# Optimization experiments

Measured on AMD Instinct MI355X. Metric: run time of the kernel, lower is better.

The kernel has to match this reference:

```python
import jax, jax.numpy as jnp
import numpy as np

N, D, K = 131072, 768, 2000


def setup_inputs() -> dict:
    key = jax.random.key(0)
    kx, kc = jax.random.split(key)
    x = jax.random.normal(kx, (N, D), dtype=jnp.float32)
    centroids = jax.random.normal(kc, (D, K), dtype=jnp.float32)  # stored as [D, K] like the torch module
    return {"x": x, "centroids": centroids}


def reference(x, centroids):
    # dist[n,k] = ||x_n||^2 - 2 x_n . c_k + ||c_k||^2  (matmul trick)
    x_norm = jnp.sum(x * x, axis=1, keepdims=True)              # [N, 1]
    c_norm = jnp.sum(centroids * centroids, axis=0, keepdims=True)  # [1, K]
    dist = x_norm - 2.0 * jnp.matmul(x, centroids) + c_norm     # [N, K]
    return jnp.argmin(dist, axis=-1)                            # [N] int
```

## Files before the change

kernel.cpp:

```cpp
#include <hip/hip_runtime.h>
#include <hip/hip_bf16.h>

#define N_ROWS 131072
#define DIM    768
#define K_C    2000
#define K_PAD  2048
#define TAU    0.2f
#define LISTCAP 8192

typedef _Float16 f16;
typedef _Float16 f16x4 __attribute__((ext_vector_type(4)));
typedef _Float16 f16x8 __attribute__((ext_vector_type(8)));
typedef float    f32x4 __attribute__((ext_vector_type(4)));

#define OFF_CN   6291456
#define OFF_XN   6299648
#define OFF_PMIN 6823936
#define OFF_PSEC 15212544
#define OFF_PIDX 23601152
#define OFF_CNT  31989760
#define OFF_LIST 31990016
#define OFF_CN64 32022784
#define OFF_XH   32039168

static __device__ __forceinline__ void gload16(const void* g, void* l) {
  __builtin_amdgcn_global_load_lds(
      (const __attribute__((address_space(1))) unsigned int*)g,
      (__attribute__((address_space(3))) unsigned int*)l, 16, 0, 0);
}

__global__ __launch_bounds__(256) void prep_cn(const float* __restrict__ cent,
                                               float* __restrict__ cn,
                                               double* __restrict__ cn64) {
#pragma clang fp contract(off)
  __shared__ float pf[8][32];
  __shared__ double pd[8][32];
  int t = threadIdx.x;
  int kk = t & 31;
  int k = blockIdx.x * 32 + kk;
  int p = t >> 5;
  float s = 0.0f;
  double s64 = 0.0;
  for (int d = p * 96; d < p * 96 + 96; ++d) {
    float c = (k < K_C) ? cent[d * K_C + k] : 0.0f;
    float sq = c * c;
    s = s + sq;
    s64 += (double)c * (double)c;
  }
  pf[p][kk] = s;
  pd[p][kk] = s64;
  __syncthreads();
  if (p == 0) {
    float ss = 0.0f;
    double ss64 = 0.0;
#pragma unroll
    for (int q = 0; q < 8; ++q) {
      ss = ss + pf[q][kk];
      ss64 += pd[q][kk];
    }
    cn[k] = (k < K_C) ? ss : INFINITY;
    cn64[k] = (k < K_C) ? ss64 : (double)INFINITY;
  }
}

__global__ __launch_bounds__(256) void prep_ct(const float* __restrict__ cent,
                                               f16* __restrict__ cTh) {
  __shared__ float ld[64][65];
  int k0 = blockIdx.x * 64;
  int d0 = blockIdx.y * 64;
  int tid = threadIdx.x;
#pragma unroll
  for (int it = 0; it < 16; ++it) {
    int idx = it * 256 + tid;
    int dd = idx >> 6, kk = idx & 63;
    int k = k0 + kk;
    ld[dd][kk] = (k < K_C) ? cent[(size_t)(d0 + dd) * K_C + k] : 0.0f;
  }
  __syncthreads();
#pragma unroll
  for (int it = 0; it < 16; ++it) {
    int idx = it * 256 + tid;
    int kk = idx >> 6, dd = idx & 63;
    cTh[(size_t)(k0 + kk) * DIM + d0 + dd] = (f16)ld[dd][kk];
  }
}

__global__ __launch_bounds__(256) void xnorm_prepx(const float* __restrict__ x,
                                                   float* __restrict__ xn,
                                                   f16* __restrict__ xh) {
#pragma clang fp contract(off)
  __shared__ __align__(16) float buf[16 * DIM];
  int row0 = blockIdx.x * 16;
  int tid = threadIdx.x;
  const f32x4* src = (const f32x4*)(x + (size_t)row0 * DIM);
  f32x4* dst = (f32x4*)buf;
#pragma unroll
  for (int c = 0; c < 12; ++c) {
    f32x4 v = src[c * 256 + tid];
    dst[c * 256 + tid] = v;
    f16x4 hv;
#pragma unroll
    for (int j = 0; j < 4; ++j) hv[j] = (f16)v[j];
    *(f16x4*)(xh + (size_t)row0 * DIM + (size_t)(c * 256 + tid) * 4) = hv;
  }
  __syncthreads();
  int w = tid >> 6, lane = tid & 63;
  int b = lane >> 3, j = lane & 7;
#pragma unroll
  for (int rr = 0; rr < 4; ++rr) {
    int r = w * 4 + rr;
    const float* a = buf + r * DIM + 96 * b + j;
    float v0 = a[0];
    float acc = v0 * v0;
#pragma unroll
    for (int t = 1; t < 12; ++t) {
      float q = a[8 * t];
      float s = q * q;
      acc = acc + s;
    }
    float v = acc;
    { float o = __shfl_xor(v, 1);  v = v + o; }
    { float o = __shfl_xor(v, 2);  v = v + o; }
    { float o = __shfl_xor(v, 4);  v = v + o; }
    { float o = __shfl_xor(v, 8);  v = v + o; }
    { float o = __shfl_xor(v, 16); v = v + o; }
    { float o = __shfl_xor(v, 32); v = v + o; }
    if (lane == 0) xn[row0 + r] = v;
  }
}

#define STAGE(bufb, ktv)                                                       \
  do {                                                                         \
    _Pragma("unroll") for (int i_ = 0; i_ < 4; ++i_) {                         \
      int q_ = w * 4 + i_;                                                     \
      int s0_ = q_ * 1024 + lane * 16;                                         \
      int row_ = s0_ >> 7;                                                     \
      int sl_ = ((s0_ >> 4) & 7) ^ (row_ & 7);                                 \
      size_t ga_ = (size_t)(rb * 128 + row_) * DIM + (ktv) * 64 + sl_ * 8;     \
      size_t gb_ = (size_t)(pb * 128 + row_) * DIM + (ktv) * 64 + sl_ * 8;     \
      gload16(xh + ga_, ldsb + (bufb) + q_ * 1024);                            \
      gload16(cTh + gb_, ldsb + 32768 + (bufb) + q_ * 1024);                   \
    }                                                                          \
  } while (0)

__global__ __launch_bounds__(256, 2) void kmeans_main(
    const f16* __restrict__ xh, const f16* __restrict__ cTh,
    const float* __restrict__ cn, const float* __restrict__ xn,
    float* __restrict__ pmin, float* __restrict__ psec,
    int* __restrict__ pidx) {
  __shared__ __align__(16) f16 lds[32768];
  char* ldsb = (char*)lds;

  int d0 = blockIdx.x;
  int g  = (d0 & 7) * 2048 + (d0 >> 3);
  int pb = g & 15;
  int rb = g >> 4;

  int tid  = threadIdx.x;
  int w    = tid >> 6;
  int lane = tid & 63;
  int wrow = (w >> 1) * 64;
  int wcol = (w & 1) * 64;

  int rsel = lane & 15;
  int ksel = lane >> 4;
  int rs0 = ((ksel ^ (rsel & 7))) << 4;
  int rs1 = (((4 + ksel) ^ (rsel & 7))) << 4;

  f32x4 acc[4][4] = {};

  STAGE(0, 0);

  for (int kt = 0; kt < 12; ++kt) {
    int bufb = (kt & 1) * 16384;
    asm volatile("s_waitcnt vmcnt(0)" ::: "memory");
    __builtin_amdgcn_sched_barrier(0);
    __builtin_amdgcn_s_barrier();
    __builtin_amdgcn_sched_barrier(0);

    if (kt < 11) STAGE(bufb ^ 16384, kt + 1);

    f16x8 ah[2][4], bh[2][4];
#pragma unroll
    for (int m = 0; m < 4; ++m) {
      int rbase = bufb + (wrow + m * 16 + rsel) * 128;
      ah[0][m] = *(const f16x8*)(ldsb + rbase + rs0);
      ah[1][m] = *(const f16x8*)(ldsb + rbase + rs1);
    }
#pragma unroll
    for (int n = 0; n < 4; ++n) {
      int rbase = bufb + 32768 + (wcol + n * 16 + rsel) * 128;
      bh[0][n] = *(const f16x8*)(ldsb + rbase + rs0);
      bh[1][n] = *(const f16x8*)(ldsb + rbase + rs1);
    }
    __builtin_amdgcn_s_setprio(1);
#pragma unroll
    for (int k32 = 0; k32 < 2; ++k32)
#pragma unroll
      for (int m = 0; m < 4; ++m)
#pragma unroll
        for (int n = 0; n < 4; ++n)
          acc[m][n] = __builtin_amdgcn_mfma_f32_16x16x32_f16(
              ah[k32][m], bh[k32][n], acc[m][n], 0, 0, 0);
    __builtin_amdgcn_s_setprio(0);
  }

  __syncthreads();
  float* lv = (float*)lds;
  float* lsv = (float*)lds + 256;
  int*   li = (int*)((float*)lds + 512);

  int colbase = pb * 128 + wcol + rsel;
  float cnv[4];
#pragma unroll
  for (int n = 0; n < 4; ++n) cnv[n] = cn[colbase + n * 16];
  int g4 = ksel * 4;

#pragma unroll
  for (int m = 0; m < 4; ++m) {
#pragma unroll
    for (int j = 0; j < 4; ++j) {
      int trow = wrow + m * 16 + g4 + j;
      float xv = xn[rb * 128 + trow];
      float v1 = 0.0f, v2 = INFINITY;
      int i1 = 0;
#pragma unroll
      for (int n = 0; n < 4; ++n) {
        float dd = (xv - 2.0f * acc[m][n][j]) + cnv[n];
        int ci = colbase + n * 16;
        if (n == 0) { v1 = dd; i1 = ci; }
        else if (dd < v1) { v2 = v1; v1 = dd; i1 = ci; }
        else { v2 = fminf(v2, dd); }
      }
#pragma unroll
      for (int off = 1; off < 16; off <<= 1) {
        float ov1 = __shfl_xor(v1, off);
        float ov2 = __shfl_xor(v2, off);
        int oi1 = __shfl_xor(i1, off);
        if (ov1 < v1 || (ov1 == v1 && oi1 < i1)) {
          v2 = fminf(v1, ov2); v1 = ov1; i1 = oi1;
        } else {
          v2 = fminf(v2, ov1);
        }
      }
      if ((lane & 15) == 0) {
        lv[(w & 1) * 128 + trow] = v1;
        lsv[(w & 1) * 128 + trow] = v2;
        li[(w & 1) * 128 + trow] = i1;
      }
    }
  }
  __syncthreads();
  if (tid < 128) {
    float a1 = lv[tid], a2 = lsv[tid];
    int aj = li[tid];
    float b1 = lv[128 + tid], b2 = lsv[128 + tid];
    int bj = li[128 + tid];
    float v1, v2; int i1;
    if (b1 < a1 || (b1 == a1 && bj < aj)) { v1 = b1; i1 = bj; v2 = fminf(b2, a1); }
    else { v1 = a1; i1 = aj; v2 = fminf(a2, b1); }
    size_t o = (size_t)pb * N_ROWS + rb * 128 + tid;
    pmin[o] = v1;
    psec[o] = v2;
    pidx[o] = i1;
  }
}

__global__ void merge_detect(const float* __restrict__ pmin,
                             const float* __restrict__ psec,
                             const int* __restrict__ pidx, int* __restrict__ out,
                             int* __restrict__ list, int* __restrict__ counter) {
  int n = blockIdx.x * 256 + threadIdx.x;
  float v1 = INFINITY, v2 = INFINITY;
  int i1 = 0x7fffffff;
  for (int p = 0; p < 16; ++p) {
    float a1 = pmin[(size_t)p * N_ROWS + n];
    float a2 = psec[(size_t)p * N_ROWS + n];
    int aj = pidx[(size_t)p * N_ROWS + n];
    if (a1 < v1 || (a1 == v1 && aj < i1)) {
      v2 = fminf(v1, a2); v1 = a1; i1 = aj;
    } else {
      v2 = fminf(v2, a1);
    }
  }
  out[n] = i1;
  if (v2 - v1 < TAU) {
    int idx = atomicAdd(counter, 1);
    if (idx < LISTCAP) list[idx] = n;
  }
}

#define ACCS(R) \
  double a##R##0 = 0, a##R##1 = 0, a##R##2 = 0, a##R##3 = 0, \
         a##R##4 = 0, a##R##5 = 0, a##R##6 = 0, a##R##7 = 0
#define FMAS(R, XV) \
  a##R##0 = fma(XV, c0, a##R##0); a##R##1 = fma(XV, c1, a##R##1); \
  a##R##2 = fma(XV, c2, a##R##2); a##R##3 = fma(XV, c3, a##R##3); \
  a##R##4 = fma(XV, c4, a##R##4); a##R##5 = fma(XV, c5, a##R##5); \
  a##R##6 = fma(XV, c6, a##R##6); a##R##7 = fma(XV, c7, a##R##7)
#define EVAL(R)                                                         \
  {                                                                     \
    double dots[8] = {a##R##0, a##R##1, a##R##2, a##R##3,               \
                      a##R##4, a##R##5, a##R##6, a##R##7};              \
    double bv = (double)INFINITY;                                       \
    int bi = 0x7fffffff;                                                \
    _Pragma("unroll") for (int j = 0; j < 8; ++j) {                     \
      int k = tid + j * 256;                                            \
      if (k < K_C) {                                                    \
        double dd = (xnorms[R] - 2.0 * dots[j]) + cn64[k];              \
        if (dd < bv) { bv = dd; bi = k; }                               \
      }                                                                 \
    }                                                                   \
    rv[tid] = bv; ri[tid] = bi;                                         \
    __syncthreads();                                                    \
    for (int s = 128; s > 0; s >>= 1) {                                 \
      if (tid < s) {                                                    \
        double ov = rv[tid + s];                                        \
        int oi = ri[tid + s];                                           \
        if (ov < rv[tid] || (ov == rv[tid] && oi < ri[tid])) {          \
          rv[tid] = ov; ri[tid] = oi;                                   \
        }                                                               \
      }                                                                 \
      __syncthreads();                                                  \
    }                                                                   \
    if (tid == 0 && (R) < nrows) out[list[b0 + (R)]] = ri[0];           \
    __syncthreads();                                                    \
  }

__global__ __launch_bounds__(256) void exact_recheck64(
    const float* __restrict__ x, const float* __restrict__ cent,
    const double* __restrict__ cn64, const int* __restrict__ list,
    const int* __restrict__ counter, int* __restrict__ out) {
  __shared__ __align__(16) float xrow[4][DIM];
  __shared__ double rv[256];
  __shared__ int ri[256];
  __shared__ double xnorms[4];
  int cnt = counter[0];
  if (cnt > LISTCAP) cnt = LISTCAP;
  int b0 = blockIdx.x * 4;
  if (b0 >= cnt) return;
  int nrows = cnt - b0;
  if (nrows > 4) nrows = 4;
  int tid = threadIdx.x;
  for (int r = 0; r < 4; ++r) {
    int n = list[b0 + (r < nrows ? r : 0)];
    double part = 0.0;
    for (int d = tid; d < DIM; d += 256) {
      float v = x[(size_t)n * DIM + d];
      xrow[r][d] = v;
      part += (double)v * (double)v;
    }
    rv[tid] = part;
    __syncthreads();
    for (int s = 128; s > 0; s >>= 1) {
      if (tid < s) rv[tid] += rv[tid + s];
      __syncthreads();
    }
    if (tid == 0) xnorms[r] = rv[0];
    __syncthreads();
  }

  int k7 = tid + 1792;
  int k7c = (k7 < K_C) ? k7 : (K_C - 1);
  ACCS(0); ACCS(1); ACCS(2); ACCS(3);
#pragma unroll 2
  for (int d = 0; d < DIM; ++d) {
    const float* cp = cent + (size_t)d * K_C + tid;
    double c0 = cp[0], c1 = cp[256], c2 = cp[512], c3 = cp[768];
    double c4 = cp[1024], c5 = cp[1280], c6 = cp[1536];
    double c7 = cp[k7c - tid];
    double x0 = xrow[0][d], x1 = xrow[1][d];
    double x2 = xrow[2][d], x3 = xrow[3][d];
    FMAS(0, x0); FMAS(1, x1); FMAS(2, x2); FMAS(3, x3);
  }
  EVAL(0) EVAL(1) EVAL(2) EVAL(3)
}

extern "C" void kernel_launch(void* const* d_in, const int* in_sizes, int n_in,
                              void* d_out, int out_size, void* d_ws, size_t ws_size,
                              hipStream_t stream) {
  const float* x = (const float*)d_in[0];
  const float* cent = (const float*)d_in[1];
  char* ws = (char*)d_ws;
  f16* cTh = (f16*)ws;
  float* cn = (float*)(ws + OFF_CN);
  float* xn = (float*)(ws + OFF_XN);
  float* pmin = (float*)(ws + OFF_PMIN);
  float* psec = (float*)(ws + OFF_PSEC);
  int* pidx = (int*)(ws + OFF_PIDX);
  int* counter = (int*)(ws + OFF_CNT);
  int* list = (int*)(ws + OFF_LIST);
  double* cn64 = (double*)(ws + OFF_CN64);
  f16* xh = (f16*)(ws + OFF_XH);

  hipMemsetAsync(counter, 0, 4, stream);
  prep_cn<<<64, 256, 0, stream>>>(cent, cn, cn64);
  prep_ct<<<dim3(32, 12), 256, 0, stream>>>(cent, cTh);
  xnorm_prepx<<<N_ROWS / 16, 256, 0, stream>>>(x, xn, xh);
  kmeans_main<<<16384, 256, 0, stream>>>(xh, cTh, cn, xn, pmin, psec, pidx);
  merge_detect<<<N_ROWS / 256, 256, 0, stream>>>(pmin, psec, pidx, (int*)d_out,
                                                 list, counter);
  exact_recheck64<<<LISTCAP / 4, 256, 0, stream>>>(x, cent, cn64, list, counter,
                                                   (int*)d_out);
}
```

Measured before the change: 1.287 ms.

## Triple-buffer K=32 tiles with lookahead-2 prefetch and three blocks per CU

Replaces the two-stage, K=64-per-step double buffer with a three-stage ring of K=32 tiles in LDS. Two tiles are prefetched ahead, and the wait uses vmcnt(4) so one stage's loads can still be in flight while MFMAs run. LDS per block drops from 64KB to 48KB and launch bounds rise to 3 blocks per CU, aiming for more latency hiding and occupancy. The XOR swizzle is dropped in favour of a plain 64-byte row layout, which may bring LDS bank conflicts, and there are twice as many barriers per K.

```diff
diff --git a/kernel.cpp b/kernel.cpp
--- a/kernel.cpp
+++ b/kernel.cpp
@@ -129,26 +129,25 @@
   }
 }
 
-#define STAGE(bufb, ktv)                                                       \
+#define STAGE3(bufo, ktv)                                                      \
   do {                                                                         \
-    _Pragma("unroll") for (int i_ = 0; i_ < 4; ++i_) {                         \
-      int q_ = w * 4 + i_;                                                     \
-      int s0_ = q_ * 1024 + lane * 16;                                         \
-      int row_ = s0_ >> 7;                                                     \
-      int sl_ = ((s0_ >> 4) & 7) ^ (row_ & 7);                                 \
-      size_t ga_ = (size_t)(rb * 128 + row_) * DIM + (ktv) * 64 + sl_ * 8;     \
-      size_t gb_ = (size_t)(pb * 128 + row_) * DIM + (ktv) * 64 + sl_ * 8;     \
-      gload16(xh + ga_, ldsb + (bufb) + q_ * 1024);                            \
-      gload16(cTh + gb_, ldsb + 32768 + (bufb) + q_ * 1024);                   \
+    _Pragma("unroll") for (int i_ = 0; i_ < 2; ++i_) {                         \
+      int c_ = w * 2 + i_;                                                     \
+      size_t ga_ = (size_t)(rb * 128 + c_ * 16 + (lane >> 2)) * DIM +          \
+                   (ktv) * 32 + (lane & 3) * 8;                                \
+      size_t gb_ = (size_t)(pb * 128 + c_ * 16 + (lane >> 2)) * DIM +          \
+                   (ktv) * 32 + (lane & 3) * 8;                                \
+      gload16(xh + ga_, ldsb + (bufo) + c_ * 1024);                            \
+      gload16(cTh + gb_, ldsb + 24576 + (bufo) + c_ * 1024);                   \
     }                                                                          \
   } while (0)
 
-__global__ __launch_bounds__(256, 2) void kmeans_main(
+__global__ __launch_bounds__(256, 3) void kmeans_main(
     const f16* __restrict__ xh, const f16* __restrict__ cTh,
     const float* __restrict__ cn, const float* __restrict__ xn,
     float* __restrict__ pmin, float* __restrict__ psec,
     int* __restrict__ pidx) {
-  __shared__ __align__(16) f16 lds[32768];
+  __shared__ __align__(16) f16 lds[24576];
   char* ldsb = (char*)lds;
 
   int d0 = blockIdx.x;
@@ -164,45 +163,46 @@
 
   int rsel = lane & 15;
   int ksel = lane >> 4;
-  int rs0 = ((ksel ^ (rsel & 7))) << 4;
-  int rs1 = (((4 + ksel) ^ (rsel & 7))) << 4;
 
   f32x4 acc[4][4] = {};
 
-  STAGE(0, 0);
-
-  for (int kt = 0; kt < 12; ++kt) {
-    int bufb = (kt & 1) * 16384;
-    asm volatile("s_waitcnt vmcnt(0)" ::: "memory");
+  STAGE3(0, 0);
+  STAGE3(8192, 1);
+
+  int cb = 0;
+  int sb = 16384;
+#pragma unroll 3
+  for (int kt = 0; kt < 24; ++kt) {
+    if (kt < 23) {
+      asm volatile("s_waitcnt vmcnt(4)" ::: "memory");
+    } else {
+      asm volatile("s_waitcnt vmcnt(0)" ::: "memory");
+    }
     __builtin_amdgcn_sched_barrier(0);
     __builtin_amdgcn_s_barrier();
     __builtin_amdgcn_sched_barrier(0);
 
-    if (kt < 11) STAGE(bufb ^ 16384, kt + 1);
-
-    f16x8 ah[2][4], bh[2][4];
-#pragma unroll
-    for (int m = 0; m < 4; ++m) {
-      int rbase = bufb + (wrow + m * 16 + rsel) * 128;
-      ah[0][m] = *(const f16x8*)(ldsb + rbase + rs0);
-      ah[1][m] = *(const f16x8*)(ldsb + rbase + rs1);
-    }
-#pragma unroll
-    for (int n = 0; n < 4; ++n) {
-      int rbase = bufb + 32768 + (wcol + n * 16 + rsel) * 128;
-      bh[0][n] = *(const f16x8*)(ldsb + rbase + rs0);
-      bh[1][n] = *(const f16x8*)(ldsb + rbase + rs1);
-    }
+    if (kt < 22) STAGE3(sb, kt + 2);
+
+    f16x8 ah[4], bh[4];
+    int abase = cb + (wrow + rsel) * 64 + ksel * 16;
+    int bbase = cb + 24576 + (wcol + rsel) * 64 + ksel * 16;
+#pragma unroll
+    for (int m = 0; m < 4; ++m) ah[m] = *(const f16x8*)(ldsb + abase + m * 1024);
+#pragma unroll
+    for (int n = 0; n < 4; ++n) bh[n] = *(const f16x8*)(ldsb + bbase + n * 1024);
+
     __builtin_amdgcn_s_setprio(1);
 #pragma unroll
-    for (int k32 = 0; k32 < 2; ++k32)
-#pragma unroll
-      for (int m = 0; m < 4; ++m)
-#pragma unroll
-        for (int n = 0; n < 4; ++n)
-          acc[m][n] = __builtin_amdgcn_mfma_f32_16x16x32_f16(
-              ah[k32][m], bh[k32][n], acc[m][n], 0, 0, 0);
+    for (int m = 0; m < 4; ++m)
+#pragma unroll
+      for (int n = 0; n < 4; ++n)
+        acc[m][n] = __builtin_amdgcn_mfma_f32_16x16x32_f16(ah[m], bh[n],
+                                                           acc[m][n], 0, 0, 0);
     __builtin_amdgcn_s_setprio(0);
+
+    cb = (cb == 16384) ? 0 : cb + 8192;
+    sb = (sb == 16384) ? 0 : sb + 8192;
   }
 
   __syncthreads();
```

Result: faster. 1.127 ms (-12.4%).
